# Kernel optimization log

Hardware: AMD Instinct MI355X
Metric: run time of the kernel (lower is better)

## Reference

```python
import jax, jax.numpy as jnp
import numpy as np

B, L, E, H, RR, BIO, NT, V, R = 16, 128, 256, 256, 128, 64, 3, 30000, 25


def setup_inputs() -> dict:
    key = jax.random.key(0)
    ks = jax.random.split(key, 24)
    s = 0.05
    n = jax.random.normal
    inp = {
        'tokens': jax.random.randint(ks[0], (B, L), 0, V),
        'bio_gold': jax.random.randint(ks[1], (B, L), 0, NT),
        'selection_gold': jax.random.uniform(ks[2], (B, L, R, L), jnp.float32),
        'word_emb': n(ks[3], (V, E), jnp.float32) * s,
        'W_ih_f': n(ks[4], (4 * H, E), jnp.float32) * s,
        'W_hh_f': n(ks[5], (4 * H, H), jnp.float32) * s,
        'b_f': n(ks[6], (4 * H,), jnp.float32) * s,
        'W_ih_b': n(ks[7], (4 * H, E), jnp.float32) * s,
        'W_hh_b': n(ks[8], (4 * H, H), jnp.float32) * s,
        'b_b': n(ks[9], (4 * H,), jnp.float32) * s,
        'emi_W': n(ks[10], (NT, H), jnp.float32) * s,
        'emi_b': n(ks[11], (NT,), jnp.float32) * s,
        'bio_emb': n(ks[12], (NT + 1, BIO), jnp.float32) * s,
        'sel_u_W': n(ks[13], (RR, H + BIO), jnp.float32) * s,
        'sel_u_b': n(ks[14], (RR,), jnp.float32) * s,
        'sel_v_W': n(ks[15], (RR, H + BIO), jnp.float32) * s,
        'sel_v_b': n(ks[16], (RR,), jnp.float32) * s,
        'sel_uv_W': n(ks[17], (RR, 2 * RR), jnp.float32) * s,
        'sel_uv_b': n(ks[18], (RR,), jnp.float32) * s,
        'rel_emb': n(ks[19], (R, RR), jnp.float32) * s,
        'crf_start': n(ks[20], (NT,), jnp.float32) * s,
        'crf_end': n(ks[21], (NT,), jnp.float32) * s,
        'crf_trans': n(ks[22], (NT, NT), jnp.float32) * s,
    }
    return inp


def _lstm(x, W_ih, W_hh, b, reverse):
    # x: [B,L,E] -> hidden states [B,L,H]; PyTorch gate order i,f,g,o
    Bb = x.shape[0]
    Hh = W_hh.shape[1]
    xg = jnp.swapaxes(jnp.einsum('ble,ge->blg', x, W_ih) + b, 0, 1)  # [L,B,4H]

    def step(carry, xt):
        h, c = carry
        g = xt + h @ W_hh.T
        i, f, gg, o = jnp.split(g, 4, axis=-1)
        c = jax.nn.sigmoid(f) * c + jax.nn.sigmoid(i) * jnp.tanh(gg)
        h = jax.nn.sigmoid(o) * jnp.tanh(c)
        return (h, c), h

    init = (jnp.zeros((Bb, Hh), x.dtype), jnp.zeros((Bb, Hh), x.dtype))
    _, hs = jax.lax.scan(step, init, xg, reverse=reverse)
    return jnp.swapaxes(hs, 0, 1)


def reference(tokens, bio_gold, selection_gold, word_emb, W_ih_f, W_hh_f, b_f,
              W_ih_b, W_hh_b, b_b, emi_W, emi_b, bio_emb, sel_u_W, sel_u_b,
              sel_v_W, sel_v_b, sel_uv_W, sel_uv_b, rel_emb, crf_start,
              crf_end, crf_trans):
    mask = tokens != 0  # pad id 0
    maskf = mask.astype(jnp.float32)
    emb = word_emb[tokens]
    # BiLSTM, halves averaged as in (fwd + bwd) / 2
    o = (_lstm(emb, W_ih_f, W_hh_f, b_f, False)
         + _lstm(emb, W_ih_b, W_hh_b, b_b, True)) * 0.5
    emi = o @ emi_W.T + emi_b  # [B,L,NT]

    # ---- CRF negative log-likelihood (torchcrf, reduction='mean') ----
    bidx = jnp.arange(tokens.shape[0])
    e_sel = jnp.take_along_axis(emi, bio_gold[..., None], axis=2)[..., 0]  # [B,L]
    num = crf_start[bio_gold[:, 0]] + e_sel[:, 0]
    tr = crf_trans[bio_gold[:, :-1], bio_gold[:, 1:]]  # [B,L-1]
    num = num + ((tr + e_sel[:, 1:]) * maskf[:, 1:]).sum(1)
    seq_ends = jnp.maximum(mask.sum(1) - 1, 0)
    num = num + crf_end[bio_gold[bidx, seq_ends]]

    def crf_step(score, inp):
        emi_t, m_t = inp
        nxt = jax.nn.logsumexp(score[:, :, None] + crf_trans[None] + emi_t[:, None, :], axis=1)
        return jnp.where(m_t[:, None], nxt, score), None

    score0 = crf_start + emi[:, 0]
    score, _ = jax.lax.scan(crf_step, score0,
                            (jnp.swapaxes(emi[:, 1:], 0, 1), jnp.swapaxes(mask[:, 1:], 0, 1)))
    den = jax.nn.logsumexp(score + crf_end, axis=1)
    crf_loss = -(num - den).mean()

    # ---- pairwise biaffine selection head ----
    oc = jnp.concatenate([o, bio_emb[bio_gold]], axis=-1)  # [B,L,H+BIO]
    u = jax.nn.relu(oc @ sel_u_W.T + sel_u_b)  # [B,L,RR]
    v = jax.nn.relu(oc @ sel_v_W.T + sel_v_b)
    Rr = rel_emb.shape[1]
    W1, W2 = sel_uv_W[:, :Rr], sel_uv_W[:, Rr:]  # split cat([u,v]) linear
    a = u @ W1.T  # indexed by j (u was expanded along dim 1)
    c = v @ W2.T  # indexed by i
    uv = jax.nn.relu(a[:, None, :, :] + c[:, :, None, :] + sel_uv_b)  # [B,L,L,RR]
    logits = jnp.einsum('bijh,rh->birj', uv, rel_emb)  # [B,L,R,L]

    y = selection_gold
    bce = jnp.maximum(logits, 0) - logits * y + jnp.log1p(jnp.exp(-jnp.abs(logits)))
    selmask = maskf[:, :, None, None] * maskf[:, None, None, :]  # [B,L,1,L]
    sel_loss = (bce * selmask).sum() / maskf.sum()
    return crf_loss + sel_loss
```

## Files before the change

### kernel.cpp

```cpp
#include <hip/hip_runtime.h>
#include <cstdint>
#include <cstddef>


typedef __attribute__((ext_vector_type(8))) short short8;
typedef __attribute__((ext_vector_type(8))) int i32x8;
typedef __attribute__((ext_vector_type(4))) float f32x4;

__device__ __forceinline__ unsigned short f2bf(float f) {
  unsigned int u = __float_as_uint(f);
  u += 0x7fffu + ((u >> 16) & 1u);
  return (unsigned short)(u >> 16);
}
__device__ __forceinline__ float bf2f(unsigned short u) {
  return __uint_as_float(((unsigned int)u) << 16);
}

__device__ __forceinline__ void dev_pp8k128(const float* __restrict__ W,
                                            unsigned int* __restrict__ out, int idx) {
  int c = idx & 3;
  int lane = (idx >> 2) & 63;
  int f = idx >> 8;
  int nt = f >> 1, kt = f & 1;
  int n = nt * 16 + (lane & 15);
  int k0 = kt * 128 + (lane >> 4) * 32 + c * 8;
  const float* wp = &W[(size_t)n * 256 + k0];
  int lo = 0, hi = 0;
  lo = __builtin_amdgcn_cvt_pk_fp8_f32(wp[0], wp[1], lo, false);
  lo = __builtin_amdgcn_cvt_pk_fp8_f32(wp[2], wp[3], lo, true);
  hi = __builtin_amdgcn_cvt_pk_fp8_f32(wp[4], wp[5], hi, false);
  hi = __builtin_amdgcn_cvt_pk_fp8_f32(wp[6], wp[7], hi, true);
  size_t base = ((size_t)(f << 6) + lane) * 8 + (c << 1);
  out[base] = (unsigned)lo;
  out[base + 1] = (unsigned)hi;
}

__device__ __forceinline__ void dev_ppw(const float* __restrict__ W, int ldw, int nkt,
                                        uint4* __restrict__ out, int idx) {
  int lane = idx & 63;
  int f = idx >> 6;
  int kt = f % nkt;
  int nt = f / nkt;
  int row = nt * 16 + (lane & 15);
  int k0 = kt * 32 + ((lane >> 4) << 3);
  const float* wp = &W[(size_t)row * ldw + k0];
  union { unsigned short us[8]; uint4 v; } tmp;
#pragma unroll
  for (int j = 0; j < 8; ++j) tmp.us[j] = f2bf(wp[j]);
  out[idx] = tmp.v;
}

__global__ __launch_bounds__(256) void k_setup(
    const float* __restrict__ Whhf, unsigned int* __restrict__ wpk8f,
    const float* __restrict__ Whhb, unsigned int* __restrict__ wpk8b,
    const float* __restrict__ Wihf, uint4* __restrict__ wihfPk,
    const float* __restrict__ Wihb, uint4* __restrict__ wihbPk,
    const float* __restrict__ suW, uint4* __restrict__ suPk,
    const float* __restrict__ svW, uint4* __restrict__ svPk,
    const float* __restrict__ suvW, uint4* __restrict__ w1Pk, uint4* __restrict__ w2Pk,
    float* __restrict__ acc) {
  int bid = blockIdx.x;
  int t = threadIdx.x;
  if (bid < 128) {
    dev_pp8k128(Whhf, wpk8f, bid * 256 + t);
  } else if (bid < 256) {
    dev_pp8k128(Whhb, wpk8b, (bid - 128) * 256 + t);
  } else if (bid < 384) {
    dev_ppw(Wihf, 256, 8, wihfPk, (bid - 256) * 256 + t);
  } else if (bid < 512) {
    dev_ppw(Wihb, 256, 8, wihbPk, (bid - 384) * 256 + t);
  } else if (bid < 532) {
    dev_ppw(suW, 320, 10, suPk, (bid - 512) * 256 + t);
  } else if (bid < 552) {
    dev_ppw(svW, 320, 10, svPk, (bid - 532) * 256 + t);
  } else if (bid < 560) {
    dev_ppw(suvW, 256, 4, w1Pk, (bid - 552) * 256 + t);
  } else if (bid < 568) {
    dev_ppw(suvW + 128, 256, 4, w2Pk, (bid - 560) * 256 + t);
  } else {
    if (t < 16) acc[t] = 0.f;
  }
}

__global__ __launch_bounds__(256) void k_xg(
    const int* __restrict__ tok, const float* __restrict__ wemb,
    const uint4* __restrict__ WpkF, const float* __restrict__ biasF,
    unsigned short* __restrict__ PF,
    const uint4* __restrict__ WpkB, const float* __restrict__ biasB,
    unsigned short* __restrict__ PB) {
  const uint4* Wp = blockIdx.y ? WpkB : WpkF;
  const float* bi = blockIdx.y ? biasB : biasF;
  unsigned short* Po = blockIdx.y ? PB : PF;
  __shared__ __align__(16) unsigned short oc[16][1024];
  int r0 = blockIdx.x * 16;
  int tid = threadIdx.x;
  int w = tid >> 6;
  int lane = tid & 63;
  int m = lane & 15;
  int q = lane >> 4;
  const float* ew = wemb + (size_t)tok[r0 + m] * 256 + (q << 3);
  f32x4 z = {0.f, 0.f, 0.f, 0.f};
  f32x4 ac[16] = {z, z, z, z, z, z, z, z, z, z, z, z, z, z, z, z};
  for (int kt = 0; kt < 8; ++kt) {
    float4 e0 = *reinterpret_cast<const float4*>(ew + (kt << 5));
    float4 e1 = *reinterpret_cast<const float4*>(ew + (kt << 5) + 4);
    union { unsigned short us[8]; short8 v; } af;
    af.us[0] = f2bf(e0.x); af.us[1] = f2bf(e0.y); af.us[2] = f2bf(e0.z); af.us[3] = f2bf(e0.w);
    af.us[4] = f2bf(e1.x); af.us[5] = f2bf(e1.y); af.us[6] = f2bf(e1.z); af.us[7] = f2bf(e1.w);
#pragma unroll
    for (int j = 0; j < 16; ++j) {
      int nt = (w << 4) + j;
      uint4 b4 = Wp[(size_t)(nt * 8 + kt) * 64 + lane];
      ac[j] = __builtin_amdgcn_mfma_f32_16x16x32_bf16(af.v, __builtin_bit_cast(short8, b4), ac[j], 0, 0, 0);
    }
  }
#pragma unroll
  for (int j = 0; j < 16; ++j) {
    int col = (w << 8) + (j << 4) + m;
    float bv = bi[col];
    int cellp = ((j >> 1) << 4) | m;
    int sub = (w << 1) | (j & 1);
#pragma unroll
    for (int reg = 0; reg < 4; ++reg) {
      int row = (q << 2) + reg;
      oc[row][(cellp << 3) + sub] = f2bf(ac[j][reg] + bv);
    }
  }
  __syncthreads();
  int b = r0 >> 7;
  unsigned short* Pb = Po + ((size_t)b << 17);
#pragma unroll
  for (int i = 0; i < 8; ++i) {
    int idx = i * 256 + tid;
    int row = idx >> 7;
    int c8 = idx & 127;
    uint4 v = *reinterpret_cast<const uint4*>(&oc[row][c8 << 3]);
    int t = (r0 + row) & 127;
    *reinterpret_cast<uint4*>(Pb + ((size_t)t << 10) + (c8 << 3)) = v;
  }
}

__global__ __launch_bounds__(512, 2) void k_lstm(
    const unsigned short* __restrict__ Pf, const unsigned short* __restrict__ Pb,
    const unsigned int* __restrict__ wpkf, const unsigned int* __restrict__ wpkb,
    unsigned short* __restrict__ hsf, unsigned short* __restrict__ hsb) {
  int bid = blockIdx.x;
  int dir = bid >> 4;
  int b = bid & 15;
  const unsigned short* P = (dir ? Pb : Pf) + ((size_t)b << 17);
  const unsigned int* wpk = dir ? wpkb : wpkf;
  unsigned short* hseq = (dir ? hsb : hsf) + (size_t)b * 128 * 256;

  __shared__ __align__(16) unsigned char h8[2][272];

  int tid = threadIdx.x;
  int w = tid >> 6;
  int lane = tid & 63;
  int m = lane & 15;
  int q = lane >> 4;
  int nsel = q & 1;
  int jj = (w << 5) + m + (nsel << 4);

  i32x8 wfr[4][2][2];
#pragma unroll
  for (int g = 0; g < 4; ++g)
#pragma unroll
    for (int n = 0; n < 2; ++n)
#pragma unroll
      for (int kt = 0; kt < 2; ++kt) {
        int f = (((g << 4) + (w << 1) + n) << 1) + kt;
        wfr[g][n][kt] = *reinterpret_cast<const i32x8*>(wpk + (((size_t)(f << 6) + lane) << 3));
      }
#pragma unroll
  for (int g = 0; g < 4; ++g)
#pragma unroll
    for (int n = 0; n < 2; ++n)
#pragma unroll
      for (int kt = 0; kt < 2; ++kt)
        asm volatile("" : "+v"(wfr[g][n][kt]));

  if (tid < 136) reinterpret_cast<unsigned int*>(&h8[0][0])[tid] = 0u;
  __syncthreads();

  const f32x4 zero4 = {0.f, 0.f, 0.f, 0.f};
  float cst = 0.f;

  auto load_x = [&](int s) -> uint4 {
    int t = dir ? (127 - (s & 127)) : (s & 127);
    return *reinterpret_cast<const uint4*>(
        P + ((size_t)((t << 7) + (w << 4) + m) << 3));
  };

  auto step = [&](int s, uint4 x4) {
    int t = dir ? (127 - s) : s;
    const unsigned char* cur = &h8[s & 1][0];
    unsigned char* nxt = &h8[(s & 1) ^ 1][0];

    i32x8 afr[2];
#pragma unroll
    for (int kt = 0; kt < 2; ++kt) {
      union { uint4 u[2]; i32x8 v; } tmp;
      const unsigned char* hp = cur + kt * 128 + q * 32;
      tmp.u[0] = *reinterpret_cast<const uint4*>(hp);
      tmp.u[1] = *reinterpret_cast<const uint4*>(hp + 16);
      afr[kt] = tmp.v;
    }

    f32x4 acg[4][2];
#pragma unroll
    for (int n = 0; n < 2; ++n) {
#pragma unroll
      for (int g = 0; g < 4; ++g)
        acg[g][n] = __builtin_amdgcn_mfma_scale_f32_16x16x128_f8f6f4(
            afr[0], wfr[g][n][0], zero4, 0, 0, 0, 0x7f7f7f7f, 0, 0x7f7f7f7f);
#pragma unroll
      for (int g = 0; g < 4; ++g)
        acg[g][n] = __builtin_amdgcn_mfma_scale_f32_16x16x128_f8f6f4(
            afr[1], wfr[g][n][1], acg[g][n], 0, 0, 0, 0x7f7f7f7f, 0, 0x7f7f7f7f);
    }

    {
      unsigned u0 = x4.x, u1 = x4.y, u2 = x4.z, u3 = x4.w;
      float x0 = __uint_as_float(nsel ? (u0 & 0xffff0000u) : (u0 << 16));
      float x1 = __uint_as_float(nsel ? (u1 & 0xffff0000u) : (u1 << 16));
      float x2 = __uint_as_float(nsel ? (u2 & 0xffff0000u) : (u2 << 16));
      float x3 = __uint_as_float(nsel ? (u3 & 0xffff0000u) : (u3 << 16));
      float gi = (nsel ? acg[0][1][0] : acg[0][0][0]) + x0;
      float gf = (nsel ? acg[1][1][0] : acg[1][0][0]) + x1;
      float gg = (nsel ? acg[2][1][0] : acg[2][0][0]) + x2;
      float go = (nsel ? acg[3][1][0] : acg[3][0][0]) + x3;
      float si = __fdividef(1.f, 1.f + __expf(-gi));
      float sf = __fdividef(1.f, 1.f + __expf(-gf));
      float so = __fdividef(1.f, 1.f + __expf(-go));
      float tg = 1.f - __fdividef(2.f, __expf(2.f * gg) + 1.f);
      float cc = sf * cst + si * tg;
      cst = cc;
      float th = 1.f - __fdividef(2.f, __expf(2.f * cc) + 1.f);
      float h = so * th;
      if (q < 2) {
        hseq[(size_t)t * 256 + jj] = f2bf(h);
        int pk = __builtin_amdgcn_cvt_pk_fp8_f32(h, h, 0, false);
        nxt[jj] = (unsigned char)(pk & 0xff);
      }
    }
    asm volatile("s_waitcnt lgkmcnt(0)" ::: "memory");
    __builtin_amdgcn_s_barrier();
    asm volatile("" ::: "memory");
  };

  uint4 xA = load_x(0);
  for (int sp = 0; sp < 128; sp += 2) {
    uint4 xB = load_x(sp + 1);
    step(sp, xA);
    xA = load_x(sp + 2);
    step(sp + 1, xB);
  }
}

__global__ __launch_bounds__(256) void k_mid2(
    const unsigned short* __restrict__ hf16, const unsigned short* __restrict__ hb16,
    const int* __restrict__ bio, const float* __restrict__ bioE,
    const float* __restrict__ emiW, const float* __restrict__ emib,
    const uint4* __restrict__ suPk, const float* __restrict__ sub,
    const uint4* __restrict__ svPk, const float* __restrict__ svb,
    const uint4* __restrict__ w1Pk, const uint4* __restrict__ w2Pk,
    unsigned short* __restrict__ a16, unsigned short* __restrict__ c16,
    float* __restrict__ emi) {
  __shared__ __align__(16) unsigned short oc[16][328];
  __shared__ __align__(16) unsigned short ub[16][136];
  __shared__ __align__(16) unsigned short vb[16][136];
  int r0 = blockIdx.x * 16;
  int tid = threadIdx.x;

#pragma unroll
  for (int it = 0; it < 8; ++it) {
    int i = it * 256 + tid;
    int row = i >> 7, h2 = (i & 127) << 1;
    unsigned int af = *reinterpret_cast<const unsigned int*>(hf16 + (size_t)(r0 + row) * 256 + h2);
    unsigned int ab = *reinterpret_cast<const unsigned int*>(hb16 + (size_t)(r0 + row) * 256 + h2);
    float lo = 0.5f * (bf2f((unsigned short)af) + bf2f((unsigned short)ab));
    float hi = 0.5f * (bf2f((unsigned short)(af >> 16)) + bf2f((unsigned short)(ab >> 16)));
    unsigned int pk = (unsigned int)f2bf(lo) | ((unsigned int)f2bf(hi) << 16);
    *reinterpret_cast<unsigned int*>(&oc[row][h2]) = pk;
  }
#pragma unroll
  for (int it = 0; it < 2; ++it) {
    int i = it * 256 + tid;
    int row = i >> 5, p = (i & 31) << 1;
    int bi = bio[r0 + row];
    float b0 = bioE[bi * 64 + p], b1 = bioE[bi * 64 + p + 1];
    unsigned int pk = (unsigned int)f2bf(b0) | ((unsigned int)f2bf(b1) << 16);
    *reinterpret_cast<unsigned int*>(&oc[row][256 + p]) = pk;
  }
  __syncthreads();

  if (tid < 192) {
    int did = tid >> 2, sub4 = tid & 3;
    int row = did / 3, g = did - row * 3;
    const float* ew = emiW + g * 256 + sub4 * 64;
    float av = 0.f;
#pragma unroll
    for (int k = 0; k < 64; ++k) av += bf2f(oc[row][sub4 * 64 + k]) * ew[k];
    av += __shfl_xor(av, 1);
    av += __shfl_xor(av, 2);
    if (sub4 == 0) emi[(size_t)(r0 + row) * 3 + g] = av + emib[g];
  }

  int w = tid >> 6, lane = tid & 63, m = lane & 15, q = lane >> 4;
  {
    f32x4 z = {0.f, 0.f, 0.f, 0.f};
    f32x4 au[2] = {z, z}, av2[2] = {z, z};
    for (int kt = 0; kt < 10; ++kt) {
      uint4 a4 = *reinterpret_cast<const uint4*>(&oc[m][(kt << 5) + (q << 3)]);
      short8 af = __builtin_bit_cast(short8, a4);
#pragma unroll
      for (int d = 0; d < 2; ++d) {
        int nt = (w << 1) + d;
        uint4 bu = suPk[(size_t)(nt * 10 + kt) * 64 + lane];
        uint4 bv = svPk[(size_t)(nt * 10 + kt) * 64 + lane];
        au[d] = __builtin_amdgcn_mfma_f32_16x16x32_bf16(af, __builtin_bit_cast(short8, bu), au[d], 0, 0, 0);
        av2[d] = __builtin_amdgcn_mfma_f32_16x16x32_bf16(af, __builtin_bit_cast(short8, bv), av2[d], 0, 0, 0);
      }
    }
#pragma unroll
    for (int d = 0; d < 2; ++d) {
      int col = ((w << 1) + d) * 16 + m;
      float bu = sub[col], bv = svb[col];
#pragma unroll
      for (int reg = 0; reg < 4; ++reg) {
        int row = (q << 2) + reg;
        ub[row][col] = f2bf(fmaxf(au[d][reg] + bu, 0.f));
        vb[row][col] = f2bf(fmaxf(av2[d][reg] + bv, 0.f));
      }
    }
  }
  __syncthreads();

  {
    f32x4 z = {0.f, 0.f, 0.f, 0.f};
    f32x4 aa[2] = {z, z}, cc[2] = {z, z};
    for (int kt = 0; kt < 4; ++kt) {
      uint4 ua = *reinterpret_cast<const uint4*>(&ub[m][(kt << 5) + (q << 3)]);
      uint4 va = *reinterpret_cast<const uint4*>(&vb[m][(kt << 5) + (q << 3)]);
      short8 uf = __builtin_bit_cast(short8, ua);
      short8 vf = __builtin_bit_cast(short8, va);
#pragma unroll
      for (int d = 0; d < 2; ++d) {
        int nt = (w << 1) + d;
        uint4 b1 = w1Pk[(size_t)((nt << 2) + kt) * 64 + lane];
        uint4 b2 = w2Pk[(size_t)((nt << 2) + kt) * 64 + lane];
        aa[d] = __builtin_amdgcn_mfma_f32_16x16x32_bf16(uf, __builtin_bit_cast(short8, b1), aa[d], 0, 0, 0);
        cc[d] = __builtin_amdgcn_mfma_f32_16x16x32_bf16(vf, __builtin_bit_cast(short8, b2), cc[d], 0, 0, 0);
      }
    }
#pragma unroll
    for (int d = 0; d < 2; ++d) {
      int col = ((w << 1) + d) * 16 + m;
#pragma unroll
      for (int reg = 0; reg < 4; ++reg) {
        int row = r0 + (q << 2) + reg;
        a16[(size_t)row * 128 + col] = f2bf(aa[d][reg]);
        c16[(size_t)row * 128 + col] = f2bf(cc[d][reg]);
      }
    }
  }
}

__global__ __launch_bounds__(256) void k_loss(
    const unsigned short* __restrict__ a16, const unsigned short* __restrict__ c16,
    const float* __restrict__ suvb, const float* __restrict__ rel,
    const float* __restrict__ y, const int* __restrict__ tok,
    const float* __restrict__ emi, const int* __restrict__ bio,
    const float* __restrict__ cstart, const float* __restrict__ cend,
    const float* __restrict__ ctrans,
    float* __restrict__ acc, float* __restrict__ out) {
  int blk = blockIdx.x;
  int tid = threadIdx.x;
  if (blk < 1024) {
    __shared__ unsigned short alds[128][136];
    __shared__ float cbs[2][128];
    __shared__ float red[4];
    int b = blk >> 6;
    int ip = blk & 63;
    int hh = tid & 127;
    int half = tid >> 7;
#pragma unroll
    for (int it = 0; it < 32; ++it) {
      int idx = it * 256 + tid;
      int jrow = idx >> 6;
      int h2 = (idx & 63) << 1;
      unsigned int av = *reinterpret_cast<const unsigned int*>(
          a16 + ((size_t)(b << 7) + jrow) * 128 + h2);
      alds[h2][jrow] = (unsigned short)av;
      alds[h2 + 1][jrow] = (unsigned short)(av >> 16);
    }
    {
      int i = (ip << 1) + half;
      cbs[half][hh] = bf2f(c16[(size_t)((b << 7) + i) * 128 + hh]) + suvb[hh];
    }
    __syncthreads();
    int i = (ip << 1) + half;
    int j = hh;
    float lg[25];
#pragma unroll
    for (int r = 0; r < 25; ++r) lg[r] = 0.f;
    for (int h = 0; h < 128; ++h) {
      float av = bf2f(alds[h][j]);
      float uv = fmaxf(av + cbs[half][h], 0.f);
#pragma unroll
      for (int r = 0; r < 25; ++r) lg[r] += uv * rel[r * 128 + h];
    }
    float mi = (tok[(b << 7) + i] != 0) ? 1.f : 0.f;
    float mj = (tok[(b << 7) + j] != 0) ? 1.f : 0.f;
    const float* yp = y + (size_t)((b << 7) + i) * 3200 + j;
    float bs = 0.f;
#pragma unroll
    for (int r = 0; r < 25; ++r) {
      float x = lg[r];
      float yv = yp[r * 128];
      bs += fmaxf(x, 0.f) - x * yv + __logf(1.f + __expf(-fabsf(x)));
    }
    bs *= mi * mj;
#pragma unroll
    for (int off = 32; off; off >>= 1) bs += __shfl_down(bs, off);
    if ((tid & 63) == 0) red[tid >> 6] = bs;
    __syncthreads();
    if (tid == 0) atomicAdd(&acc[0], red[0] + red[1] + red[2] + red[3]);
  } else {
    __shared__ float elds[128][4];
    __shared__ float msk[128];
    __shared__ int biol[128];
    __shared__ float r_t[2], r_m[2];
    int b = blk - 1024;
    int t = tid;
    if (t < 128) {
      biol[t] = bio[b * 128 + t];
      msk[t] = (tok[b * 128 + t] != 0) ? 1.f : 0.f;
#pragma unroll
      for (int g = 0; g < 3; ++g) elds[t][g] = emi[(b * 128 + t) * 3 + g];
    }
    __syncthreads();
    if (t < 128) {
      float m = msk[t];
      float term;
      if (t == 0)
        term = cstart[biol[0]] + elds[0][biol[0]];
      else
        term = (ctrans[biol[t - 1] * 3 + biol[t]] + elds[t][biol[t]]) * m;
      float ms = m;
#pragma unroll
      for (int off = 32; off; off >>= 1) {
        term += __shfl_down(term, off);
        ms += __shfl_down(ms, off);
      }
      if ((t & 63) == 0) { r_t[t >> 6] = term; r_m[t >> 6] = ms; }
    }
    __syncthreads();
    if (t == 0) {
      float num = r_t[0] + r_t[1];
      float msum = r_m[0] + r_m[1];
      int se = (int)msum - 1;
      if (se < 0) se = 0;
      num += cend[biol[se]];
      float tr[9];
#pragma unroll
      for (int i2 = 0; i2 < 9; ++i2) tr[i2] = ctrans[i2];
      float s0 = cstart[0] + elds[0][0];
      float s1 = cstart[1] + elds[0][1];
      float s2 = cstart[2] + elds[0][2];
      for (int tt = 1; tt < 128; ++tt) {
        float a0, a1, a2, mx, n0, n1, n2;
        a0 = s0 + tr[0]; a1 = s1 + tr[3]; a2 = s2 + tr[6];
        mx = fmaxf(a0, fmaxf(a1, a2));
        n0 = mx + __logf(__expf(a0 - mx) + __expf(a1 - mx) + __expf(a2 - mx)) + elds[tt][0];
        a0 = s0 + tr[1]; a1 = s1 + tr[4]; a2 = s2 + tr[7];
        mx = fmaxf(a0, fmaxf(a1, a2));
        n1 = mx + __logf(__expf(a0 - mx) + __expf(a1 - mx) + __expf(a2 - mx)) + elds[tt][1];
        a0 = s0 + tr[2]; a1 = s1 + tr[5]; a2 = s2 + tr[8];
        mx = fmaxf(a0, fmaxf(a1, a2));
        n2 = mx + __logf(__expf(a0 - mx) + __expf(a1 - mx) + __expf(a2 - mx)) + elds[tt][2];
        if (msk[tt] != 0.f) { s0 = n0; s1 = n1; s2 = n2; }
      }
      float a0 = s0 + cend[0], a1 = s1 + cend[1], a2 = s2 + cend[2];
      float mx = fmaxf(a0, fmaxf(a1, a2));
      float den = mx + __logf(__expf(a0 - mx) + __expf(a1 - mx) + __expf(a2 - mx));
      atomicAdd(&acc[1], num - den);
      atomicAdd(&acc[2], msum);
    }
  }
  if (tid == 0) {
    __threadfence();
    unsigned old = atomicAdd((unsigned int*)(acc + 5), 1u);
    if (old == 1039u) {
      __threadfence();
      float s0 = atomicAdd(&acc[0], 0.f);
      float s1 = atomicAdd(&acc[1], 0.f);
      float s2 = atomicAdd(&acc[2], 0.f);
      out[0] = -(s1 * (1.f / 16.f)) + s0 / s2;
    }
  }
}

extern "C" void kernel_launch(void* const* d_in, const int* in_sizes, int n_in,
                              void* d_out, int out_size, void* d_ws, size_t ws_size,
                              hipStream_t stream) {
  const int* tokens = (const int*)d_in[0];
  const int* bio = (const int*)d_in[1];
  const float* selg = (const float*)d_in[2];
  const float* wemb = (const float*)d_in[3];
  const float* Wihf = (const float*)d_in[4];
  const float* Whhf = (const float*)d_in[5];
  const float* bf = (const float*)d_in[6];
  const float* Wihb = (const float*)d_in[7];
  const float* Whhb = (const float*)d_in[8];
  const float* bb = (const float*)d_in[9];
  const float* emiW = (const float*)d_in[10];
  const float* emib = (const float*)d_in[11];
  const float* bioE = (const float*)d_in[12];
  const float* suW = (const float*)d_in[13];
  const float* sub = (const float*)d_in[14];
  const float* svW = (const float*)d_in[15];
  const float* svb = (const float*)d_in[16];
  const float* suvW = (const float*)d_in[17];
  const float* suvb = (const float*)d_in[18];
  const float* rel = (const float*)d_in[19];
  const float* cstart = (const float*)d_in[20];
  const float* cend = (const float*)d_in[21];
  const float* ctrans = (const float*)d_in[22];

  float* ws = (float*)d_ws;
  float* xgf16 = ws;
  float* xgb16 = xgf16 + 1048576;
  float* hf16 = xgb16 + 1048576;
  float* hb16 = hf16 + 262144;
  float* a16 = hb16 + 262144;
  float* c16 = a16 + 131072;
  float* emi = c16 + 131072;
  float* wpk8f = emi + 6144;
  float* wpk8b = wpk8f + 65536;
  float* wihfPk = wpk8b + 65536;
  float* wihbPk = wihfPk + 131072;
  float* suPk = wihbPk + 131072;
  float* svPk = suPk + 20480;
  float* w1Pk = svPk + 20480;
  float* w2Pk = w1Pk + 8192;
  float* acc = w2Pk + 8192;

  k_setup<<<569, 256, 0, stream>>>(
      Whhf, (unsigned int*)wpk8f, Whhb, (unsigned int*)wpk8b,
      Wihf, (uint4*)wihfPk, Wihb, (uint4*)wihbPk,
      suW, (uint4*)suPk, svW, (uint4*)svPk,
      suvW, (uint4*)w1Pk, (uint4*)w2Pk, acc);

  k_xg<<<dim3(128, 2), 256, 0, stream>>>(
      tokens, wemb,
      (const uint4*)wihfPk, bf, (unsigned short*)xgf16,
      (const uint4*)wihbPk, bb, (unsigned short*)xgb16);

  k_lstm<<<32, 512, 0, stream>>>(
      (const unsigned short*)xgf16, (const unsigned short*)xgb16,
      (const unsigned int*)wpk8f, (const unsigned int*)wpk8b,
      (unsigned short*)hf16, (unsigned short*)hb16);

  k_mid2<<<128, 256, 0, stream>>>(
      (const unsigned short*)hf16, (const unsigned short*)hb16,
      bio, bioE, emiW, emib,
      (const uint4*)suPk, sub, (const uint4*)svPk, svb,
      (const uint4*)w1Pk, (const uint4*)w2Pk,
      (unsigned short*)a16, (unsigned short*)c16, emi);

  k_loss<<<1040, 256, 0, stream>>>((const unsigned short*)a16, (const unsigned short*)c16,
                                   suvb, rel, selg, tokens, emi, bio,
                                   cstart, cend, ctrans, acc, (float*)d_out);
}
```

Measured before the change: 348.3 us.

## Split LSTM recurrence barrier into two half-K phases across warp groups

```diff
diff --git a/kernel.cpp b/kernel.cpp
--- a/kernel.cpp
+++ b/kernel.cpp
@@ -160,6 +160,7 @@
   int q = lane >> 4;
   int nsel = q & 1;
   int jj = (w << 5) + m + (nsel << 4);
+  bool lowg = (w < 4);
 
   i32x8 wfr[4][2][2];
 #pragma unroll
@@ -191,20 +192,47 @@
         P + ((size_t)((t << 7) + (w << 4) + m) << 3));
   };
 
+  i32x8 afr0, afr1;
+  {
+    const unsigned char* cur = &h8[0][0];
+    union { uint4 u[2]; i32x8 v; } t0, t1;
+    t0.u[0] = *reinterpret_cast<const uint4*>(cur + q * 32);
+    t0.u[1] = *reinterpret_cast<const uint4*>(cur + q * 32 + 16);
+    t1.u[0] = *reinterpret_cast<const uint4*>(cur + 128 + q * 32);
+    t1.u[1] = *reinterpret_cast<const uint4*>(cur + 128 + q * 32 + 16);
+    afr0 = t0.v;
+    afr1 = t1.v;
+  }
+
+  auto gates = [&](const f32x4 acg[4][2], uint4 x4, int t,
+                   unsigned char* nxt) {
+    unsigned u0 = x4.x, u1 = x4.y, u2 = x4.z, u3 = x4.w;
+    float x0 = __uint_as_float(nsel ? (u0 & 0xffff0000u) : (u0 << 16));
+    float x1 = __uint_as_float(nsel ? (u1 & 0xffff0000u) : (u1 << 16));
+    float x2 = __uint_as_float(nsel ? (u2 & 0xffff0000u) : (u2 << 16));
+    float x3 = __uint_as_float(nsel ? (u3 & 0xffff0000u) : (u3 << 16));
+    float gi = (nsel ? acg[0][1][0] : acg[0][0][0]) + x0;
+    float gf = (nsel ? acg[1][1][0] : acg[1][0][0]) + x1;
+    float gg = (nsel ? acg[2][1][0] : acg[2][0][0]) + x2;
+    float go = (nsel ? acg[3][1][0] : acg[3][0][0]) + x3;
+    float si = __fdividef(1.f, 1.f + __expf(-gi));
+    float sf = __fdividef(1.f, 1.f + __expf(-gf));
+    float so = __fdividef(1.f, 1.f + __expf(-go));
+    float tg = 1.f - __fdividef(2.f, __expf(2.f * gg) + 1.f);
+    float cc = sf * cst + si * tg;
+    cst = cc;
+    float th = 1.f - __fdividef(2.f, __expf(2.f * cc) + 1.f);
+    float h = so * th;
+    if (q < 2) {
+      hseq[(size_t)t * 256 + jj] = f2bf(h);
+      int pk = __builtin_amdgcn_cvt_pk_fp8_f32(h, h, 0, false);
+      nxt[jj] = (unsigned char)(pk & 0xff);
+    }
+  };
+
   auto step = [&](int s, uint4 x4) {
     int t = dir ? (127 - s) : s;
-    const unsigned char* cur = &h8[s & 1][0];
     unsigned char* nxt = &h8[(s & 1) ^ 1][0];
-
-    i32x8 afr[2];
-#pragma unroll
-    for (int kt = 0; kt < 2; ++kt) {
-      union { uint4 u[2]; i32x8 v; } tmp;
-      const unsigned char* hp = cur + kt * 128 + q * 32;
-      tmp.u[0] = *reinterpret_cast<const uint4*>(hp);
-      tmp.u[1] = *reinterpret_cast<const uint4*>(hp + 16);
-      afr[kt] = tmp.v;
-    }
 
     f32x4 acg[4][2];
 #pragma unroll
@@ -212,40 +240,46 @@
 #pragma unroll
       for (int g = 0; g < 4; ++g)
         acg[g][n] = __builtin_amdgcn_mfma_scale_f32_16x16x128_f8f6f4(
-            afr[0], wfr[g][n][0], zero4, 0, 0, 0, 0x7f7f7f7f, 0, 0x7f7f7f7f);
+            afr0, wfr[g][n][0], zero4, 0, 0, 0, 0x7f7f7f7f, 0, 0x7f7f7f7f);
 #pragma unroll
       for (int g = 0; g < 4; ++g)
         acg[g][n] = __builtin_amdgcn_mfma_scale_f32_16x16x128_f8f6f4(
-            afr[1], wfr[g][n][1], acg[g][n], 0, 0, 0, 0x7f7f7f7f, 0, 0x7f7f7f7f);
-    }
-
-    {
-      unsigned u0 = x4.x, u1 = x4.y, u2 = x4.z, u3 = x4.w;
-      float x0 = __uint_as_float(nsel ? (u0 & 0xffff0000u) : (u0 << 16));
-      float x1 = __uint_as_float(nsel ? (u1 & 0xffff0000u) : (u1 << 16));
-      float x2 = __uint_as_float(nsel ? (u2 & 0xffff0000u) : (u2 << 16));
-      float x3 = __uint_as_float(nsel ? (u3 & 0xffff0000u) : (u3 << 16));
-      float gi = (nsel ? acg[0][1][0] : acg[0][0][0]) + x0;
-      float gf = (nsel ? acg[1][1][0] : acg[1][0][0]) + x1;
-      float gg = (nsel ? acg[2][1][0] : acg[2][0][0]) + x2;
-      float go = (nsel ? acg[3][1][0] : acg[3][0][0]) + x3;
-      float si = __fdividef(1.f, 1.f + __expf(-gi));
-      float sf = __fdividef(1.f, 1.f + __expf(-gf));
-      float so = __fdividef(1.f, 1.f + __expf(-go));
-      float tg = 1.f - __fdividef(2.f, __expf(2.f * gg) + 1.f);
-      float cc = sf * cst + si * tg;
-      cst = cc;
-      float th = 1.f - __fdividef(2.f, __expf(2.f * cc) + 1.f);
-      float h = so * th;
-      if (q < 2) {
-        hseq[(size_t)t * 256 + jj] = f2bf(h);
-        int pk = __builtin_amdgcn_cvt_pk_fp8_f32(h, h, 0, false);
-        nxt[jj] = (unsigned char)(pk & 0xff);
-      }
-    }
-    asm volatile("s_waitcnt lgkmcnt(0)" ::: "memory");
-    __builtin_amdgcn_s_barrier();
-    asm volatile("" ::: "memory");
+            afr1, wfr[g][n][1], acg[g][n], 0, 0, 0, 0x7f7f7f7f, 0, 0x7f7f7f7f);
+    }
+
+    if (lowg) {
+      gates(acg, x4, t, nxt);
+      asm volatile("s_waitcnt lgkmcnt(0)" ::: "memory");
+      __builtin_amdgcn_s_barrier();
+      asm volatile("" ::: "memory");
+      union { uint4 u[2]; i32x8 v; } t0;
+      t0.u[0] = *reinterpret_cast<const uint4*>(nxt + q * 32);
+      t0.u[1] = *reinterpret_cast<const uint4*>(nxt + q * 32 + 16);
+      asm volatile("" ::: "memory");
+      __builtin_amdgcn_s_barrier();
+      asm volatile("" ::: "memory");
+      union { uint4 u[2]; i32x8 v; } t1;
+      t1.u[0] = *reinterpret_cast<const uint4*>(nxt + 128 + q * 32);
+      t1.u[1] = *reinterpret_cast<const uint4*>(nxt + 128 + q * 32 + 16);
+      afr0 = t0.v;
+      afr1 = t1.v;
+    } else {
+      asm volatile("" ::: "memory");
+      __builtin_amdgcn_s_barrier();
+      asm volatile("" ::: "memory");
+      union { uint4 u[2]; i32x8 v; } t0;
+      t0.u[0] = *reinterpret_cast<const uint4*>(nxt + q * 32);
+      t0.u[1] = *reinterpret_cast<const uint4*>(nxt + q * 32 + 16);
+      gates(acg, x4, t, nxt);
+      asm volatile("s_waitcnt lgkmcnt(0)" ::: "memory");
+      __builtin_amdgcn_s_barrier();
+      asm volatile("" ::: "memory");
+      union { uint4 u[2]; i32x8 v; } t1;
+      t1.u[0] = *reinterpret_cast<const uint4*>(nxt + 128 + q * 32);
+      t1.u[1] = *reinterpret_cast<const uint4*>(nxt + 128 + q * 32 + 16);
+      afr0 = t0.v;
+      afr1 = t1.v;
+    }
   };
 
   uint4 xA = load_x(0);
```

Measured after the change: 350.9 us. About the same (+0.7%).
